# Performance work log

Measured on AMD Instinct MI355X. Metric: run time of the kernel, lower is better.

Reference implementation:

```python
import math
import jax, jax.numpy as jnp
import numpy as np

ALPHA = 0.7

def setup_inputs() -> dict:
    key = jax.random.key(0)
    ks = jax.random.split(key, 4)
    T, V, Q, F, D = 256, 256, 32, 64, 512
    return {
        "text_embed": jax.random.normal(ks[0], (T, D), dtype=jnp.float32),
        "clip_embed": jax.random.normal(ks[1], (V, D), dtype=jnp.float32),
        "concept_embeds": jax.random.normal(ks[2], (T, Q, D), dtype=jnp.float32),
        "frame_embeds": jax.random.normal(ks[3], (V, F, D), dtype=jnp.float32),
        "logit_scale": jnp.array(math.log(1.0 / 0.07), dtype=jnp.float32),
    }

def _l2norm(x, eps=1e-12):
    # matches F.normalize(dim=-1): x / max(||x||, eps)
    n = jnp.sqrt(jnp.sum(x * x, axis=-1, keepdims=True))
    return x / jnp.maximum(n, eps)

def reference(text_embed, clip_embed, concept_embeds, frame_embeds, logit_scale):
    scale = jnp.minimum(jnp.exp(logit_scale), 100.0)
    # global similarity: [T, V]
    g_sim = scale * (text_embed @ clip_embed.T)
    # local MaxSim: normalize, dot products, max over frames f, mean over tokens q
    nc = _l2norm(concept_embeds.astype(jnp.float32))  # [T, Q, D]
    nf = _l2norm(frame_embeds.astype(jnp.float32))    # [V, F, D]
    scores = jnp.einsum('tqd,vfd->tvqf', nc, nf)      # [T, V, Q, F]
    max_scores = jnp.max(scores, axis=-1)             # [T, V, Q]
    l_sim = scale * jnp.mean(max_scores, axis=-1)     # [T, V]
    return ALPHA * g_sim + (1.0 - ALPHA) * l_sim
```

## Files before the change

kernel.cpp:

```cpp
#include <hip/hip_runtime.h>
#include <stdint.h>

#define ALPHA_ 0.7f
constexpr int Tn = 256, Vn = 256, Qn = 32, Fn = 64, Dn = 512;
constexpr int Mn = Tn * Qn;
constexpr int Nn = Vn * Fn;
constexpr int Kn = Dn;
constexpr int NOT = 8;
constexpr int GT  = (Kn / 64) * NOT;

typedef float  f32x4  __attribute__((ext_vector_type(4)));
typedef __bf16 bf16x8 __attribute__((ext_vector_type(8)));

static __device__ __forceinline__ unsigned short f2bf(float f) {
  uint32_t x = __builtin_bit_cast(uint32_t, f);
  x += 0x7fffu + ((x >> 16) & 1u);
  return (unsigned short)(x >> 16);
}

static __device__ __forceinline__ void gload_lds16(const void* g, void* l) {
  __builtin_amdgcn_global_load_lds(
      (const __attribute__((address_space(1))) uint32_t*)g,
      (__attribute__((address_space(3))) uint32_t*)l, 16, 0, 0);
}

#define BAR()   asm volatile("s_barrier" ::: "memory")
#define SBAR()  __builtin_amdgcn_sched_barrier(0)
#define LGKM(N) do { asm volatile("s_waitcnt lgkmcnt(" #N ")" ::: "memory"); \
                     SBAR(); } while (0)
#define VM6()   asm volatile("s_waitcnt vmcnt(6)" ::: "memory")
#define VM0()   asm volatile("s_waitcnt vmcnt(0)" ::: "memory")

__global__ void normalize_rows(const float* __restrict__ src,
                               uint4* __restrict__ dst) {
  const int wave = threadIdx.x >> 6;
  const int lane = threadIdx.x & 63;
  const int row  = blockIdx.x * 4 + wave;
  const float4* p = reinterpret_cast<const float4*>(src + (size_t)row * Dn + lane * 8);
  float4 x0 = p[0];
  float4 x1 = p[1];
  float ss = x0.x*x0.x + x0.y*x0.y + x0.z*x0.z + x0.w*x0.w
           + x1.x*x1.x + x1.y*x1.y + x1.z*x1.z + x1.w*x1.w;
  #pragma unroll
  for (int m = 1; m < 64; m <<= 1) ss += __shfl_xor(ss, m, 64);
  const float inv = 1.0f / fmaxf(sqrtf(ss), 1e-12f);
  union { unsigned short u[8]; uint4 v; } pk;
  const float f[8] = {x0.x, x0.y, x0.z, x0.w, x1.x, x1.y, x1.z, x1.w};
  #pragma unroll
  for (int j = 0; j < 8; ++j) pk.u[j] = f2bf(f[j] * inv);
  dst[(size_t)row * (Dn / 8) + lane] = pk.v;
}

__global__ __launch_bounds__(512, 2)
void maxsim256_kernel(const uint16_t* __restrict__ Abf,
                      const uint16_t* __restrict__ Bbf,
                      const float* __restrict__ text,
                      const float* __restrict__ clip,
                      const float* __restrict__ logit_scale,
                      float* __restrict__ out) {
  __shared__ __align__(16) unsigned char lds[131072];
  const int tid  = threadIdx.x;
  const int lane = tid & 63;
  const int wave = tid >> 6;
  const int wr   = wave >> 2;
  const int wc   = wave & 3;
  const int bid  = blockIdx.x;
  const int nx0  = (bid & 7) * 8;
  const int by   = bid >> 3;

  const float scale = fminf(expf(logit_scale[0]), 100.0f);
  const float coefG = ALPHA_ * scale;
  const float coefL = (1.0f - ALPHA_) * scale * (1.0f / (float)Qn);

  const char* Ag  = reinterpret_cast<const char*>(Abf) + (size_t)by  * 262144;
  const char* Bg0 = reinterpret_cast<const char*>(Bbf) + (size_t)nx0 * 262144;

  unsigned srcA[2], srcB[2], ldsoff[2];
  #pragma unroll
  for (int j = 0; j < 2; ++j) {
    const unsigned r = (j * 8 + wave) * 8 + (lane >> 3);
    const unsigned c = (((lane & 7) ^ (lane >> 3)) << 4);
    srcA[j]  = (((r >> 6) << 7) + (r & 63)) * 1024 + c;
    srcB[j]  = (((r >> 5) << 6) + (r & 31)) * 1024 + c;
    ldsoff[j] = (j * 8 + wave) * 1024;
  }

  auto stage = [&](int buf, int isB, int h, int g) {
    const unsigned base = buf * 65536 + isB * 32768 + h * 16384;
    const unsigned kt = (g & 7) * 128;
    #pragma unroll
    for (int j = 0; j < 2; ++j) {
      const void* src = isB
          ? (const void*)(Bg0 + (size_t)((g >> 3) * 262144 + h * 32768 + kt + srcB[j]))
          : (const void*)(Ag  + (size_t)(h * 65536 + kt + srcA[j]));
      gload_lds16(src, &lds[base + ldsoff[j]]);
    }
  };

  f32x4 acc[8][4];
  #pragma unroll
  for (int i = 0; i < 8; ++i)
    #pragma unroll
    for (int j = 0; j < 4; ++j)
      acc[i][j] = {0.f, 0.f, 0.f, 0.f};

  bf16x8 af[4][2];
  bf16x8 bq[4][2];

  const int rA  = lane & 15;
  const int kg  = lane >> 4;
  const unsigned key = (unsigned)(rA & 7) << 4;

  auto ldA = [&](int buf, int h) {
    const unsigned b = buf * 65536 + h * 16384;
    #pragma unroll
    for (int m = 0; m < 4; ++m) {
      const unsigned s = (unsigned)(wr * 64 + m * 16 + rA);
      #pragma unroll
      for (int kk = 0; kk < 2; ++kk) {
        const unsigned kb = kk * 64 + kg * 16;
        af[m][kk] = *reinterpret_cast<const bf16x8*>(&lds[b + s * 128 + (kb ^ key)]);
      }
    }
  };
  auto ldB = [&](int buf, int h) {
    const unsigned b = buf * 65536 + 32768 + h * 16384;
    #pragma unroll
    for (int n = 0; n < 2; ++n) {
      const unsigned s = (unsigned)(wc * 32 + n * 16 + rA);
      #pragma unroll
      for (int kk = 0; kk < 2; ++kk) {
        const unsigned kb = kk * 64 + kg * 16;
        bq[h * 2 + n][kk] = *reinterpret_cast<const bf16x8*>(&lds[b + s * 128 + (kb ^ key)]);
      }
    }
  };
  auto mfma_half = [&](int hm, int hn) {
    #pragma unroll
    for (int m = 0; m < 4; ++m)
      #pragma unroll
      for (int n = 0; n < 2; ++n)
        #pragma unroll
        for (int kk = 0; kk < 2; ++kk) {
          const int mi = hm * 4 + m, ni = hn * 2 + n;
          acc[mi][ni] = __builtin_amdgcn_mfma_f32_16x16x32_bf16(
              af[m][kk], bq[ni][kk], acc[mi][ni], 0, 0, 0);
        }
  };

  auto epilogue = [&](int ot) {
    const int v_out = (nx0 + ot) * 4 + wc;
    const float4* cp = reinterpret_cast<const float4*>(clip + (size_t)v_out * Dn) + lane * 2;
    const float4 c0 = cp[0], c1 = cp[1];
    #pragma unroll
    for (int gq = 0; gq < 4; ++gq) {
      float sum = 0.f;
      #pragma unroll
      for (int m2 = 0; m2 < 2; ++m2) {
        const int mi = gq * 2 + m2;
        #pragma unroll
        for (int reg = 0; reg < 4; ++reg) {
          float rm = fmaxf(fmaxf(acc[mi][0][reg], acc[mi][1][reg]),
                           fmaxf(acc[mi][2][reg], acc[mi][3][reg]));
          rm = fmaxf(rm, __shfl_xor(rm, 1, 64));
          rm = fmaxf(rm, __shfl_xor(rm, 2, 64));
          rm = fmaxf(rm, __shfl_xor(rm, 4, 64));
          rm = fmaxf(rm, __shfl_xor(rm, 8, 64));
          sum += rm;
        }
      }
      sum += __shfl_xor(sum, 16, 64);
      sum += __shfl_xor(sum, 32, 64);
      const float4* tp = reinterpret_cast<const float4*>(
          text + (size_t)(by * 8 + wr * 4 + gq) * Dn) + lane * 2;
      const float4 t0 = tp[0], t1 = tp[1];
      float gd = t0.x*c0.x + t0.y*c0.y + t0.z*c0.z + t0.w*c0.w
               + t1.x*c1.x + t1.y*c1.y + t1.z*c1.z + t1.w*c1.w;
      gd += __shfl_xor(gd, 1, 64);  gd += __shfl_xor(gd, 2, 64);
      gd += __shfl_xor(gd, 4, 64);  gd += __shfl_xor(gd, 8, 64);
      gd += __shfl_xor(gd, 16, 64); gd += __shfl_xor(gd, 32, 64);
      if (lane == 0)
        out[(by * 8 + wr * 4 + gq) * Vn + v_out] = coefG * gd + coefL * sum;
    }
    #pragma unroll
    for (int i = 0; i < 8; ++i)
      #pragma unroll
      for (int j = 0; j < 4; ++j)
        acc[i][j] = {0.f, 0.f, 0.f, 0.f};
  };

  stage(0, 0, 0, 0); stage(0, 1, 0, 0); stage(0, 1, 1, 0); stage(0, 0, 1, 0);
  stage(1, 0, 0, 1); stage(1, 1, 0, 1); stage(1, 1, 1, 1);
  VM6(); BAR();

  auto tile_step = [&](int g, int buf) {
    ldA(buf, 0); ldB(buf, 0);
    SBAR();
    ldB(buf, 1);
    SBAR();
    if (g + 1 < GT) stage(buf ^ 1, 0, 1, g + 1);
    LGKM(4);
    __builtin_amdgcn_s_setprio(1);
    mfma_half(0, 0);
    __builtin_amdgcn_s_setprio(0);
    LGKM(0);
    __builtin_amdgcn_s_setprio(1);
    mfma_half(0, 1);
    __builtin_amdgcn_s_setprio(0);
    BAR();
    ldA(buf, 1);
    SBAR();
    if (g + 2 < GT) {
      stage(buf, 0, 0, g + 2);
      stage(buf, 1, 0, g + 2);
      stage(buf, 1, 1, g + 2);
    }
    LGKM(0);
    __builtin_amdgcn_s_setprio(1);
    mfma_half(1, 1);
    mfma_half(1, 0);
    __builtin_amdgcn_s_setprio(0);
    if (g < GT - 2) { VM6(); } else { VM0(); }
    if ((g & 7) == 7) epilogue(g >> 3);
    BAR();
  };

  for (int t = 0; t < GT; t += 2) {
    tile_step(t, 0);
    tile_step(t + 1, 1);
  }
}

extern "C" void kernel_launch(void* const* d_in, const int* in_sizes, int n_in,
                              void* d_out, int out_size, void* d_ws, size_t ws_size,
                              hipStream_t stream) {
  const float* text        = (const float*)d_in[0];
  const float* clip        = (const float*)d_in[1];
  const float* concept     = (const float*)d_in[2];
  const float* frames      = (const float*)d_in[3];
  const float* logit_scale = (const float*)d_in[4];
  float* out = (float*)d_out;

  uint16_t* Abf = (uint16_t*)d_ws;
  uint16_t* Bbf = Abf + (size_t)Mn * Kn;

  normalize_rows<<<Mn / 4, 256, 0, stream>>>(concept, (uint4*)Abf);
  normalize_rows<<<Nn / 4, 256, 0, stream>>>(frames, (uint4*)Bbf);
  maxsim256_kernel<<<256, 512, 0, stream>>>(Abf, Bbf, text, clip, logit_scale, out);
}
```

Measured before the change: 221.2 us.

## Restructure GEMM main loop with register double-buffered fragments and one barrier

The per-tile schedule is rebuilt so the A and B fragments for the next K-tile are read from LDS into a second register set while the current tile's MFMAs run. The B fragments ping-pong between two register arrays, and the second A half goes into its own array. The loop drops from two barriers per tile to one, and each tile is staged as a whole with a vmcnt(0) wait before the barrier. This aims to hide LDS read latency and cut synchronization stalls, at the cost of more VGPRs (pressure at 2 waves/SIMD) and a shallower global-load wait window.

```diff
diff --git a/kernel.cpp b/kernel.cpp
--- a/kernel.cpp
+++ b/kernel.cpp
@@ -28,8 +28,8 @@
 #define SBAR()  __builtin_amdgcn_sched_barrier(0)
 #define LGKM(N) do { asm volatile("s_waitcnt lgkmcnt(" #N ")" ::: "memory"); \
                      SBAR(); } while (0)
-#define VM6()   asm volatile("s_waitcnt vmcnt(6)" ::: "memory")
-#define VM0()   asm volatile("s_waitcnt vmcnt(0)" ::: "memory")
+#define VMW(N)  do { asm volatile("s_waitcnt vmcnt(" #N ")" ::: "memory"); \
+                     SBAR(); } while (0)
 
 __global__ void normalize_rows(const float* __restrict__ src,
                                uint4* __restrict__ dst) {
@@ -96,6 +96,10 @@
       gload_lds16(src, &lds[base + ldsoff[j]]);
     }
   };
+  auto stage_tile = [&](int buf, int g) {
+    stage(buf, 0, 0, g); stage(buf, 0, 1, g);
+    stage(buf, 1, 0, g); stage(buf, 1, 1, g);
+  };
 
   f32x4 acc[8][4];
   #pragma unroll
@@ -105,13 +109,15 @@
       acc[i][j] = {0.f, 0.f, 0.f, 0.f};
 
   bf16x8 af[4][2];
-  bf16x8 bq[4][2];
+  bf16x8 af2[4][2];
+  bf16x8 bqA[4][2];
+  bf16x8 bqB[4][2];
 
   const int rA  = lane & 15;
   const int kg  = lane >> 4;
   const unsigned key = (unsigned)(rA & 7) << 4;
 
-  auto ldA = [&](int buf, int h) {
+  auto ldA_into = [&](int buf, int h, bf16x8 (&dst)[4][2]) {
     const unsigned b = buf * 65536 + h * 16384;
     #pragma unroll
     for (int m = 0; m < 4; ++m) {
@@ -119,33 +125,36 @@
       #pragma unroll
       for (int kk = 0; kk < 2; ++kk) {
         const unsigned kb = kk * 64 + kg * 16;
-        af[m][kk] = *reinterpret_cast<const bf16x8*>(&lds[b + s * 128 + (kb ^ key)]);
+        dst[m][kk] = *reinterpret_cast<const bf16x8*>(&lds[b + s * 128 + (kb ^ key)]);
       }
     }
   };
-  auto ldB = [&](int buf, int h) {
-    const unsigned b = buf * 65536 + 32768 + h * 16384;
-    #pragma unroll
-    for (int n = 0; n < 2; ++n) {
-      const unsigned s = (unsigned)(wc * 32 + n * 16 + rA);
-      #pragma unroll
-      for (int kk = 0; kk < 2; ++kk) {
-        const unsigned kb = kk * 64 + kg * 16;
-        bq[h * 2 + n][kk] = *reinterpret_cast<const bf16x8*>(&lds[b + s * 128 + (kb ^ key)]);
-      }
-    }
-  };
-  auto mfma_half = [&](int hm, int hn) {
-    #pragma unroll
-    for (int m = 0; m < 4; ++m)
-      #pragma unroll
-      for (int n = 0; n < 2; ++n)
+  auto ldB_into = [&](int buf, bf16x8 (&dst)[4][2]) {
+    #pragma unroll
+    for (int h = 0; h < 2; ++h) {
+      const unsigned b = buf * 65536 + 32768 + h * 16384;
+      #pragma unroll
+      for (int n = 0; n < 2; ++n) {
+        const unsigned s = (unsigned)(wc * 32 + n * 16 + rA);
         #pragma unroll
         for (int kk = 0; kk < 2; ++kk) {
-          const int mi = hm * 4 + m, ni = hn * 2 + n;
-          acc[mi][ni] = __builtin_amdgcn_mfma_f32_16x16x32_bf16(
-              af[m][kk], bq[ni][kk], acc[mi][ni], 0, 0, 0);
+          const unsigned kb = kk * 64 + kg * 16;
+          dst[h * 2 + n][kk] = *reinterpret_cast<const bf16x8*>(&lds[b + s * 128 + (kb ^ key)]);
         }
+      }
+    }
+  };
+  auto mfma_cluster = [&](int hm, bf16x8 (&a)[4][2], bf16x8 (&b)[4][2]) {
+    __builtin_amdgcn_s_setprio(1);
+    #pragma unroll
+    for (int m = 0; m < 4; ++m)
+      #pragma unroll
+      for (int ni = 0; ni < 4; ++ni)
+        #pragma unroll
+        for (int kk = 0; kk < 2; ++kk)
+          acc[hm * 4 + m][ni] = __builtin_amdgcn_mfma_f32_16x16x32_bf16(
+              a[m][kk], b[ni][kk], acc[hm * 4 + m][ni], 0, 0, 0);
+    __builtin_amdgcn_s_setprio(0);
   };
 
   auto epilogue = [&](int ot) {
@@ -189,45 +198,36 @@
         acc[i][j] = {0.f, 0.f, 0.f, 0.f};
   };
 
-  stage(0, 0, 0, 0); stage(0, 1, 0, 0); stage(0, 1, 1, 0); stage(0, 0, 1, 0);
-  stage(1, 0, 0, 1); stage(1, 1, 0, 1); stage(1, 1, 1, 1);
-  VM6(); BAR();
-
-  auto tile_step = [&](int g, int buf) {
-    ldA(buf, 0); ldB(buf, 0);
+  auto tile_step = [&](int g, int buf, bf16x8 (&bq_cur)[4][2],
+                       bf16x8 (&bq_nxt)[4][2]) {
+    ldA_into(buf, 1, af2);
     SBAR();
-    ldB(buf, 1);
-    SBAR();
-    if (g + 1 < GT) stage(buf ^ 1, 0, 1, g + 1);
-    LGKM(4);
-    __builtin_amdgcn_s_setprio(1);
-    mfma_half(0, 0);
-    __builtin_amdgcn_s_setprio(0);
+    LGKM(8);
+    mfma_cluster(0, af, bq_cur);
     LGKM(0);
-    __builtin_amdgcn_s_setprio(1);
-    mfma_half(0, 1);
-    __builtin_amdgcn_s_setprio(0);
+    VMW(0);
     BAR();
-    ldA(buf, 1);
-    SBAR();
-    if (g + 2 < GT) {
-      stage(buf, 0, 0, g + 2);
-      stage(buf, 1, 0, g + 2);
-      stage(buf, 1, 1, g + 2);
-    }
-    LGKM(0);
-    __builtin_amdgcn_s_setprio(1);
-    mfma_half(1, 1);
-    mfma_half(1, 0);
-    __builtin_amdgcn_s_setprio(0);
-    if (g < GT - 2) { VM6(); } else { VM0(); }
+    if (g + 1 < GT) {
+      ldA_into(buf ^ 1, 0, af);
+      ldB_into(buf ^ 1, bq_nxt);
+      SBAR();
+    }
+    if (g + 2 < GT) stage_tile(buf, g + 2);
+    mfma_cluster(1, af2, bq_cur);
     if ((g & 7) == 7) epilogue(g >> 3);
-    BAR();
-  };
+  };
+
+  stage_tile(0, 0);
+  stage_tile(1, 1);
+  VMW(8);
+  BAR();
+  ldA_into(0, 0, af);
+  ldB_into(0, bqA);
+  SBAR();
 
   for (int t = 0; t < GT; t += 2) {
-    tile_step(t, 0);
-    tile_step(t + 1, 1);
+    tile_step(t,     0, bqA, bqB);
+    tile_step(t + 1, 1, bqB, bqA);
   }
 }
 
```

Result: slower. 676.3 us (+205.8%).

## Switch MaxSim GEMM from 16x16x32 to 32x32x16 bf16 MFMA tiles

Applied to the files above, without the earlier changes.

Replaces the 16x16x32 MFMA fragments with 32x32x16 bf16 MFMAs. This reshapes the accumulator layout into four-by-two 16-wide vectors and changes the LDS fragment loads to match. The larger MFMA halves the number of LDS fragment reads per FLOP and the instruction count, but changes the epilogue max-reduction to a 32-lane shuffle pattern. A separate A-fragment register set is added for the second half, which raises register pressure under the 512x2 launch bounds.

```diff
diff --git a/kernel.cpp b/kernel.cpp
--- a/kernel.cpp
+++ b/kernel.cpp
@@ -9,7 +9,7 @@
 constexpr int NOT = 8;
 constexpr int GT  = (Kn / 64) * NOT;
 
-typedef float  f32x4  __attribute__((ext_vector_type(4)));
+typedef float  f32x16 __attribute__((ext_vector_type(16)));
 typedef __bf16 bf16x8 __attribute__((ext_vector_type(8)));
 
 static __device__ __forceinline__ unsigned short f2bf(float f) {
@@ -97,82 +97,82 @@
     }
   };
 
-  f32x4 acc[8][4];
-  #pragma unroll
-  for (int i = 0; i < 8; ++i)
-    #pragma unroll
-    for (int j = 0; j < 4; ++j)
-      acc[i][j] = {0.f, 0.f, 0.f, 0.f};
-
-  bf16x8 af[4][2];
-  bf16x8 bq[4][2];
-
-  const int rA  = lane & 15;
-  const int kg  = lane >> 4;
-  const unsigned key = (unsigned)(rA & 7) << 4;
-
-  auto ldA = [&](int buf, int h) {
-    const unsigned b = buf * 65536 + h * 16384;
-    #pragma unroll
-    for (int m = 0; m < 4; ++m) {
-      const unsigned s = (unsigned)(wr * 64 + m * 16 + rA);
-      #pragma unroll
-      for (int kk = 0; kk < 2; ++kk) {
-        const unsigned kb = kk * 64 + kg * 16;
-        af[m][kk] = *reinterpret_cast<const bf16x8*>(&lds[b + s * 128 + (kb ^ key)]);
-      }
-    }
-  };
-  auto ldB = [&](int buf, int h) {
-    const unsigned b = buf * 65536 + 32768 + h * 16384;
-    #pragma unroll
-    for (int n = 0; n < 2; ++n) {
-      const unsigned s = (unsigned)(wc * 32 + n * 16 + rA);
-      #pragma unroll
-      for (int kk = 0; kk < 2; ++kk) {
-        const unsigned kb = kk * 64 + kg * 16;
-        bq[h * 2 + n][kk] = *reinterpret_cast<const bf16x8*>(&lds[b + s * 128 + (kb ^ key)]);
-      }
-    }
-  };
-  auto mfma_half = [&](int hm, int hn) {
-    #pragma unroll
-    for (int m = 0; m < 4; ++m)
-      #pragma unroll
-      for (int n = 0; n < 2; ++n)
-        #pragma unroll
-        for (int kk = 0; kk < 2; ++kk) {
-          const int mi = hm * 4 + m, ni = hn * 2 + n;
-          acc[mi][ni] = __builtin_amdgcn_mfma_f32_16x16x32_bf16(
-              af[m][kk], bq[ni][kk], acc[mi][ni], 0, 0, 0);
-        }
-  };
+  f32x16 acc[4][2];
+#define ZACC() do {                                                        \
+    _Pragma("unroll") for (int i_ = 0; i_ < 4; ++i_)                       \
+      _Pragma("unroll") for (int n_ = 0; n_ < 2; ++n_)                     \
+        _Pragma("unroll") for (int e_ = 0; e_ < 16; ++e_)                  \
+          acc[i_][n_][e_] = 0.f;                                           \
+  } while (0)
+  ZACC();
+
+  bf16x8 af[2][4];
+  bf16x8 af2[2][4];
+  bf16x8 bq[2][4];
+
+  const int l31 = lane & 31;
+  const unsigned key = (unsigned)(lane & 7) << 4;
+  unsigned ck[4];
+  #pragma unroll
+  for (int k = 0; k < 4; ++k)
+    ck[k] = (unsigned)(k * 32 + (lane >> 5) * 16) ^ key;
+  const unsigned o_a32 = (unsigned)(wr * 64 + l31) * 128;
+  const unsigned o_b32 = (unsigned)(wc * 32 + l31) * 128;
+
+#define LDA(BUF, H, DST) do {                                              \
+    const unsigned b_ = (unsigned)(BUF) * 65536 + (H) * 16384 + o_a32;     \
+    _Pragma("unroll") for (int m_ = 0; m_ < 2; ++m_)                       \
+      _Pragma("unroll") for (int k_ = 0; k_ < 4; ++k_)                     \
+        DST[m_][k_] = *reinterpret_cast<const bf16x8*>(                    \
+            &lds[b_ + m_ * 4096 + ck[k_]]);                                \
+  } while (0)
+
+#define LDB(BUF, NF) do {                                                  \
+    const unsigned b_ = (unsigned)(BUF) * 65536 + 32768 + (NF) * 16384 + o_b32; \
+    _Pragma("unroll") for (int k_ = 0; k_ < 4; ++k_)                       \
+      bq[NF][k_] = *reinterpret_cast<const bf16x8*>(&lds[b_ + ck[k_]]);    \
+  } while (0)
+
+#define HALF(HM, AF, NF) do {                                              \
+    __builtin_amdgcn_s_setprio(1);                                         \
+    _Pragma("unroll") for (int k_ = 0; k_ < 4; ++k_)                       \
+      _Pragma("unroll") for (int m_ = 0; m_ < 2; ++m_)                     \
+        acc[(HM) * 2 + m_][NF] = __builtin_amdgcn_mfma_f32_32x32x16_bf16(  \
+            AF[m_][k_], bq[NF][k_], acc[(HM) * 2 + m_][NF], 0, 0, 0);      \
+    __builtin_amdgcn_s_setprio(0);                                         \
+  } while (0)
+
+#define HALF2(HM, AF) do {                                                 \
+    __builtin_amdgcn_s_setprio(1);                                         \
+    _Pragma("unroll") for (int k_ = 0; k_ < 4; ++k_)                       \
+      _Pragma("unroll") for (int n_ = 0; n_ < 2; ++n_)                     \
+        _Pragma("unroll") for (int m_ = 0; m_ < 2; ++m_)                   \
+          acc[(HM) * 2 + m_][n_] = __builtin_amdgcn_mfma_f32_32x32x16_bf16(\
+              AF[m_][k_], bq[n_][k_], acc[(HM) * 2 + m_][n_], 0, 0, 0);    \
+    __builtin_amdgcn_s_setprio(0);                                         \
+  } while (0)
 
   auto epilogue = [&](int ot) {
     const int v_out = (nx0 + ot) * 4 + wc;
     const float4* cp = reinterpret_cast<const float4*>(clip + (size_t)v_out * Dn) + lane * 2;
     const float4 c0 = cp[0], c1 = cp[1];
     #pragma unroll
-    for (int gq = 0; gq < 4; ++gq) {
-      float sum = 0.f;
+    for (int mf = 0; mf < 4; ++mf) {
+      float s = 0.f;
       #pragma unroll
-      for (int m2 = 0; m2 < 2; ++m2) {
-        const int mi = gq * 2 + m2;
-        #pragma unroll
-        for (int reg = 0; reg < 4; ++reg) {
-          float rm = fmaxf(fmaxf(acc[mi][0][reg], acc[mi][1][reg]),
-                           fmaxf(acc[mi][2][reg], acc[mi][3][reg]));
-          rm = fmaxf(rm, __shfl_xor(rm, 1, 64));
-          rm = fmaxf(rm, __shfl_xor(rm, 2, 64));
-          rm = fmaxf(rm, __shfl_xor(rm, 4, 64));
-          rm = fmaxf(rm, __shfl_xor(rm, 8, 64));
-          sum += rm;
-        }
+      for (int j = 0; j < 16; ++j) {
+        float rm = fmaxf(acc[mf][0][j], acc[mf][1][j]);
+        rm = fmaxf(rm, __shfl_xor(rm, 1, 64));
+        rm = fmaxf(rm, __shfl_xor(rm, 2, 64));
+        rm = fmaxf(rm, __shfl_xor(rm, 4, 64));
+        rm = fmaxf(rm, __shfl_xor(rm, 8, 64));
+        rm = fmaxf(rm, __shfl_xor(rm, 16, 64));
+        s += rm;
       }
-      sum += __shfl_xor(sum, 16, 64);
-      sum += __shfl_xor(sum, 32, 64);
+      s += __shfl_xor(s, 32, 64);
+      const int t_out = by * 8 + wr * 4 + mf;
       const float4* tp = reinterpret_cast<const float4*>(
-          text + (size_t)(by * 8 + wr * 4 + gq) * Dn) + lane * 2;
+          text + (size_t)t_out * Dn) + lane * 2;
       const float4 t0 = tp[0], t1 = tp[1];
       float gd = t0.x*c0.x + t0.y*c0.y + t0.z*c0.z + t0.w*c0.w
                + t1.x*c1.x + t1.y*c1.y + t1.z*c1.z + t1.w*c1.w;
@@ -180,13 +180,9 @@
       gd += __shfl_xor(gd, 4, 64);  gd += __shfl_xor(gd, 8, 64);
       gd += __shfl_xor(gd, 16, 64); gd += __shfl_xor(gd, 32, 64);
       if (lane == 0)
-        out[(by * 8 + wr * 4 + gq) * Vn + v_out] = coefG * gd + coefL * sum;
+        out[t_out * Vn + v_out] = coefG * gd + coefL * s;
     }
-    #pragma unroll
-    for (int i = 0; i < 8; ++i)
-      #pragma unroll
-      for (int j = 0; j < 4; ++j)
-        acc[i][j] = {0.f, 0.f, 0.f, 0.f};
+    ZACC();
   };
 
   stage(0, 0, 0, 0); stage(0, 1, 0, 0); stage(0, 1, 1, 0); stage(0, 0, 1, 0);
@@ -194,21 +190,18 @@
   VM6(); BAR();
 
   auto tile_step = [&](int g, int buf) {
-    ldA(buf, 0); ldB(buf, 0);
+    LDA(buf, 0, af);
+    LDB(buf, 0);
     SBAR();
-    ldB(buf, 1);
+    LDB(buf, 1);
     SBAR();
     if (g + 1 < GT) stage(buf ^ 1, 0, 1, g + 1);
     LGKM(4);
-    __builtin_amdgcn_s_setprio(1);
-    mfma_half(0, 0);
-    __builtin_amdgcn_s_setprio(0);
+    HALF(0, af, 0);
     LGKM(0);
-    __builtin_amdgcn_s_setprio(1);
-    mfma_half(0, 1);
-    __builtin_amdgcn_s_setprio(0);
+    HALF(0, af, 1);
     BAR();
-    ldA(buf, 1);
+    LDA(buf, 1, af2);
     SBAR();
     if (g + 2 < GT) {
       stage(buf, 0, 0, g + 2);
@@ -216,10 +209,7 @@
       stage(buf, 1, 1, g + 2);
     }
     LGKM(0);
-    __builtin_amdgcn_s_setprio(1);
-    mfma_half(1, 1);
-    mfma_half(1, 0);
-    __builtin_amdgcn_s_setprio(0);
+    HALF2(1, af2);
     if (g < GT - 2) { VM6(); } else { VM0(); }
     if ((g & 7) == 7) epilogue(g >> 3);
     BAR();
```

New measurement: 258.6 us. +16.9%, slower.
